# Performance work log

Hardware: AMD Instinct MI355X
Metric: run time of the kernel (lower is better)

Reference implementation:

```python
import jax, jax.numpy as jnp
import numpy as np

N = 100000      # user + item nodes
E = 600000      # number of edges
LATDIM = 128
HEAD = 4
HDIM = LATDIM // HEAD


def setup_inputs() -> dict:
    key = jax.random.key(0)
    ks = jax.random.split(key, 7)
    return {
        "embeds": jax.random.normal(ks[0], (N, LATDIM), dtype=jnp.float32),
        "qTrans": jax.random.normal(ks[1], (LATDIM, LATDIM), dtype=jnp.float32) * (1.0 / np.sqrt(LATDIM)),
        "kTrans": jax.random.normal(ks[2], (LATDIM, LATDIM), dtype=jnp.float32) * (1.0 / np.sqrt(LATDIM)),
        "vTrans": jax.random.normal(ks[3], (LATDIM, LATDIM), dtype=jnp.float32) * (1.0 / np.sqrt(LATDIM)),
        "filt": jax.random.normal(ks[4], (N, HEAD), dtype=jnp.float32),
        "rows": jax.random.randint(ks[5], (E,), 0, N, dtype=jnp.int32),
        "cols": jax.random.randint(ks[6], (E,), 0, N, dtype=jnp.int32),
    }


def reference(embeds, qTrans, kTrans, vTrans, filt, rows, cols):
    # gather endpoint embeddings: [E, latdim]
    rowEmbeds = embeds[rows]
    colEmbeds = embeds[cols]
    # per-edge multi-head q/k/v: [E, H, D]
    qEmbeds = (rowEmbeds @ qTrans).reshape(E, HEAD, HDIM)
    kEmbeds = (colEmbeds @ kTrans).reshape(E, HEAD, HDIM)
    vEmbeds = (colEmbeds @ vTrans).reshape(E, HEAD, HDIM)
    # per-edge per-head attention logits
    att = jnp.einsum('ehd,ehd->eh', qEmbeds, kEmbeds)
    att = jnp.clip(att, -10.0, 10.0)
    att = att + filt[cols]
    expAtt = jnp.exp(att)
    # segment softmax over destination rows
    attNorm = jax.ops.segment_sum(expAtt, rows, num_segments=N)[rows]
    att = expAtt / (attNorm + 1e-8)
    # weighted values, scatter-sum back to nodes
    resEdges = (att[:, :, None] * vEmbeds).reshape(E, LATDIM)
    resEmbeds = jax.ops.segment_sum(resEdges, rows, num_segments=N)
    return resEmbeds
```

## Files before the change

### kernel.cpp

```cpp
#include <hip/hip_runtime.h>

#define N_NODES 100000
#define E_EDGES 600000
#define LATDIM 128
#define HEAD 4
#define HDIM 32

#define SCAN_CHUNK 1024
#define SCAN_NB ((N_NODES + SCAN_CHUNK - 1) / SCAN_CHUNK)

typedef __bf16 bf16x8 __attribute__((ext_vector_type(8)));
typedef float  f32x4  __attribute__((ext_vector_type(4)));

__device__ __forceinline__ unsigned f32_to_bf16_rne(float x) {
    unsigned u = __float_as_uint(x);
    u += 0x7fffu + ((u >> 16) & 1u);
    return u >> 16;
}

__device__ __forceinline__ void bf16_split(float x, unsigned& hi, unsigned& lo) {
    unsigned hb = f32_to_bf16_rne(x);
    float hf = __uint_as_float(hb << 16);
    unsigned lb = f32_to_bf16_rne(x - hf);
    hi = hb; lo = lb;
}

__global__ __launch_bounds__(256) void wprep_kernel(
    const float* __restrict__ qT, const float* __restrict__ kT,
    const float* __restrict__ vT,
    unsigned short* __restrict__ WThi, unsigned short* __restrict__ WTlo)
{
    int g = blockIdx.x * 256 + threadIdx.x;
    if (g >= 3072) return;
    int m    = g >> 10;
    int rem  = g & 1023;
    int c    = rem >> 3;
    int k0   = (rem & 7) * 16;
    const float* W = (m == 0) ? qT : (m == 1) ? kT : vT;

    unsigned short hi[16], lo[16];
    #pragma unroll
    for (int j = 0; j < 16; ++j) {
        float x = W[(size_t)(k0 + j) * 128 + c];
        unsigned hb, lb;
        bf16_split(x, hb, lb);
        hi[j] = (unsigned short)hb;
        lo[j] = (unsigned short)lb;
    }
    size_t off = (size_t)m * 16384 + (size_t)c * 128 + k0;
    *(uint4*)(WThi + off)     = *(const uint4*)&hi[0];
    *(uint4*)(WThi + off + 8) = *(const uint4*)&hi[8];
    *(uint4*)(WTlo + off)     = *(const uint4*)&lo[0];
    *(uint4*)(WTlo + off + 8) = *(const uint4*)&lo[8];
}

__global__ __launch_bounds__(256, 4) void qkv_mfma_kernel(
    const float* __restrict__ embeds,
    const unsigned short* __restrict__ WThi,
    const unsigned short* __restrict__ WTlo,
    float* __restrict__ Q, unsigned* __restrict__ KV)
{
    __shared__ __align__(16) char smem[32768];
    char* Ahi = smem;
    char* Alo = smem + 16384;
    char* Bhi = smem;
    char* Blo = smem + 16384;

    const int tid = threadIdx.x;
    const int rowBase = blockIdx.x * 64;

    uint4 pbh0, pbh1, pbh2, pbh3;
    uint4 pbl0, pbl1, pbl2, pbl3;

#define PF(MN, HN) do {                                                          \
        const char* _sh = (const char*)(WThi + (size_t)(MN) * 16384 + (size_t)(HN) * 8192); \
        const char* _sl = (const char*)(WTlo + (size_t)(MN) * 16384 + (size_t)(HN) * 8192); \
        pbh0 = *(const uint4*)(_sh + (size_t)(0 * 256 + tid) * 16);              \
        pbh1 = *(const uint4*)(_sh + (size_t)(1 * 256 + tid) * 16);              \
        pbh2 = *(const uint4*)(_sh + (size_t)(2 * 256 + tid) * 16);              \
        pbh3 = *(const uint4*)(_sh + (size_t)(3 * 256 + tid) * 16);              \
        pbl0 = *(const uint4*)(_sl + (size_t)(0 * 256 + tid) * 16);              \
        pbl1 = *(const uint4*)(_sl + (size_t)(1 * 256 + tid) * 16);              \
        pbl2 = *(const uint4*)(_sl + (size_t)(2 * 256 + tid) * 16);              \
        pbl3 = *(const uint4*)(_sl + (size_t)(3 * 256 + tid) * 16);              \
    } while (0)

#define COMMIT() do {                                                            \
        { int _i = 0 * 256 + tid; int _c = _i >> 4;                              \
          int _s = (_c * 256 + (_i & 15) * 16) ^ ((_c & 7) << 4);                \
          *(uint4*)(Bhi + _s) = pbh0; *(uint4*)(Blo + _s) = pbl0; }              \
        { int _i = 1 * 256 + tid; int _c = _i >> 4;                              \
          int _s = (_c * 256 + (_i & 15) * 16) ^ ((_c & 7) << 4);                \
          *(uint4*)(Bhi + _s) = pbh1; *(uint4*)(Blo + _s) = pbl1; }              \
        { int _i = 2 * 256 + tid; int _c = _i >> 4;                              \
          int _s = (_c * 256 + (_i & 15) * 16) ^ ((_c & 7) << 4);                \
          *(uint4*)(Bhi + _s) = pbh2; *(uint4*)(Blo + _s) = pbl2; }              \
        { int _i = 3 * 256 + tid; int _c = _i >> 4;                              \
          int _s = (_c * 256 + (_i & 15) * 16) ^ ((_c & 7) << 4);                \
          *(uint4*)(Bhi + _s) = pbh3; *(uint4*)(Blo + _s) = pbl3; }              \
    } while (0)

#define MFMA_PANEL(ACC) do {                                                     \
        _Pragma("unroll")                                                        \
        for (int kk = 0; kk < 4; ++kk) {                                         \
            _Pragma("unroll")                                                    \
            for (int n = 0; n < 4; ++n) {                                        \
                int brow = n * 16 + lrow;                                        \
                int byte = brow * 256 + kk * 64 + kg * 16;                       \
                int swz  = byte ^ ((lrow & 7) << 4);                             \
                bf16x8 bh = __builtin_bit_cast(bf16x8, *(const uint4*)(Bhi + swz)); \
                bf16x8 bl = __builtin_bit_cast(bf16x8, *(const uint4*)(Blo + swz)); \
                ACC[n] = __builtin_amdgcn_mfma_f32_16x16x32_bf16(a_hi[kk], bh, ACC[n], 0, 0, 0); \
                ACC[n] = __builtin_amdgcn_mfma_f32_16x16x32_bf16(a_lo[kk], bh, ACC[n], 0, 0, 0); \
                ACC[n] = __builtin_amdgcn_mfma_f32_16x16x32_bf16(a_hi[kk], bl, ACC[n], 0, 0, 0); \
            }                                                                    \
        }                                                                        \
    } while (0)

#define ZACC(ACC) f32x4 ACC[4] = { {0.f,0.f,0.f,0.f}, {0.f,0.f,0.f,0.f},         \
                                   {0.f,0.f,0.f,0.f}, {0.f,0.f,0.f,0.f} }

#define STORE_Q(ACC, H) do {                                                     \
        _Pragma("unroll")                                                        \
        for (int n = 0; n < 4; ++n)                                              \
        _Pragma("unroll")                                                        \
        for (int j = 0; j < 4; ++j) {                                            \
            int gr  = rowBase + wv * 16 + orow + j;                              \
            int col = (H) * 64 + n * 16 + lrow;                                  \
            if (gr < N_NODES) Q[(size_t)gr * 128 + col] = ACC[n][j];             \
        }                                                                        \
    } while (0)

#define STORE_KV(ACC, H) do {                                                    \
        _Pragma("unroll")                                                        \
        for (int n = 0; n < 4; ++n)                                              \
        _Pragma("unroll")                                                        \
        for (int j = 0; j < 4; ++j) {                                            \
            int gr  = rowBase + wv * 16 + orow + j;                              \
            int col = (H) * 64 + n * 16 + lrow;                                  \
            if (gr < N_NODES) {                                                  \
                unsigned pk = f32_to_bf16_rne(kreg[n][j])                        \
                            | (f32_to_bf16_rne(ACC[n][j]) << 16);                \
                KV[(size_t)gr * 128 + col] = pk;                                 \
            }                                                                    \
        }                                                                        \
    } while (0)

    PF(0, 0);

    #pragma unroll
    for (int it = 0; it < 8; ++it) {
        int idx = it * 256 + tid;
        int r  = idx >> 5;
        int c4 = idx & 31;
        int gr = rowBase + r;
        float4 v = make_float4(0.f, 0.f, 0.f, 0.f);
        if (gr < N_NODES) v = ((const float4*)embeds)[(size_t)gr * 32 + c4];
        unsigned hx, lx, hy, ly, hz, lz, hw, lw;
        bf16_split(v.x, hx, lx); bf16_split(v.y, hy, ly);
        bf16_split(v.z, hz, lz); bf16_split(v.w, hw, lw);
        uint2 hp = make_uint2(hx | (hy << 16), hz | (hw << 16));
        uint2 lp = make_uint2(lx | (ly << 16), lz | (lw << 16));
        int byte = r * 256 + c4 * 8;
        int swz  = byte ^ ((r & 7) << 4);
        *(uint2*)(Ahi + swz) = hp;
        *(uint2*)(Alo + swz) = lp;
    }
    __syncthreads();

    const int lane = tid & 63;
    const int wv   = tid >> 6;
    const int lrow = lane & 15;
    const int kg   = lane >> 4;
    const int arow = wv * 16 + lrow;
    const int orow = kg << 2;

    bf16x8 a_hi[4], a_lo[4];
    #pragma unroll
    for (int kk = 0; kk < 4; ++kk) {
        int byte = arow * 256 + kk * 64 + kg * 16;
        int swz  = byte ^ ((lrow & 7) << 4);
        a_hi[kk] = __builtin_bit_cast(bf16x8, *(const uint4*)(Ahi + swz));
        a_lo[kk] = __builtin_bit_cast(bf16x8, *(const uint4*)(Alo + swz));
    }
    __syncthreads();

    COMMIT();
    __syncthreads();

    f32x4 kreg[4];

    {
        PF(1, 0);
        ZACC(acc);
        MFMA_PANEL(acc);
        STORE_Q(acc, 0);
        __syncthreads(); COMMIT(); __syncthreads();
    }
    {
        PF(2, 0);
        ZACC(acc);
        MFMA_PANEL(acc);
        kreg[0] = acc[0]; kreg[1] = acc[1]; kreg[2] = acc[2]; kreg[3] = acc[3];
        __syncthreads(); COMMIT(); __syncthreads();
    }
    {
        PF(0, 1);
        ZACC(acc);
        MFMA_PANEL(acc);
        STORE_KV(acc, 0);
        __syncthreads(); COMMIT(); __syncthreads();
    }
    {
        PF(1, 1);
        ZACC(acc);
        MFMA_PANEL(acc);
        STORE_Q(acc, 1);
        __syncthreads(); COMMIT(); __syncthreads();
    }
    {
        PF(2, 1);
        ZACC(acc);
        MFMA_PANEL(acc);
        kreg[0] = acc[0]; kreg[1] = acc[1]; kreg[2] = acc[2]; kreg[3] = acc[3];
        __syncthreads(); COMMIT(); __syncthreads();
    }
    {
        ZACC(acc);
        MFMA_PANEL(acc);
        STORE_KV(acc, 1);
    }

#undef PF
#undef COMMIT
#undef MFMA_PANEL
#undef ZACC
#undef STORE_Q
#undef STORE_KV
}

__global__ __launch_bounds__(256) void hist_kernel(
    const int* __restrict__ rows, int* __restrict__ counts)
{
    int e = blockIdx.x * 256 + threadIdx.x;
    if (e < E_EDGES) atomicAdd(&counts[rows[e]], 1);
}

__global__ __launch_bounds__(256) void scan1_kernel(
    const int* __restrict__ counts, int* __restrict__ starts,
    int* __restrict__ blockSums)
{
    __shared__ int s[256];
    int b = blockIdx.x, t = threadIdx.x;
    int base = b * SCAN_CHUNK + t * 4;
    int v0 = (base + 0 < N_NODES) ? counts[base + 0] : 0;
    int v1 = (base + 1 < N_NODES) ? counts[base + 1] : 0;
    int v2 = (base + 2 < N_NODES) ? counts[base + 2] : 0;
    int v3 = (base + 3 < N_NODES) ? counts[base + 3] : 0;
    int local = v0 + v1 + v2 + v3;
    s[t] = local;
    __syncthreads();
    for (int off = 1; off < 256; off <<= 1) {
        int x = (t >= off) ? s[t - off] : 0;
        __syncthreads();
        s[t] += x;
        __syncthreads();
    }
    int incl = s[t];
    int excl = incl - local;
    if (base + 0 < N_NODES) starts[base + 0] = excl;
    if (base + 1 < N_NODES) starts[base + 1] = excl + v0;
    if (base + 2 < N_NODES) starts[base + 2] = excl + v0 + v1;
    if (base + 3 < N_NODES) starts[base + 3] = excl + v0 + v1 + v2;
    if (t == 255) blockSums[b] = incl;
}

__global__ __launch_bounds__(128) void scan2_kernel(int* __restrict__ blockSums)
{
    __shared__ int s[128];
    int t = threadIdx.x;
    int v = (t < SCAN_NB) ? blockSums[t] : 0;
    s[t] = v;
    __syncthreads();
    for (int off = 1; off < 128; off <<= 1) {
        int x = (t >= off) ? s[t - off] : 0;
        __syncthreads();
        s[t] += x;
        __syncthreads();
    }
    if (t < SCAN_NB) blockSums[t] = s[t] - v;
}

__global__ __launch_bounds__(256) void scan3_kernel(
    int* __restrict__ starts, const int* __restrict__ blockSums,
    int* __restrict__ cursor)
{
    int i = blockIdx.x * 256 + threadIdx.x;
    if (i < N_NODES) {
        int v = starts[i] + blockSums[i >> 10];
        starts[i] = v;
        cursor[i] = v;
    }
}

__global__ __launch_bounds__(256) void scatter_kernel(
    const int* __restrict__ rows, const int* __restrict__ cols,
    int* __restrict__ cursor, int* __restrict__ csrCols)
{
    int e = blockIdx.x * 256 + threadIdx.x;
    if (e >= E_EDGES) return;
    int pos = atomicAdd(&cursor[rows[e]], 1);
    csrCols[pos] = cols[e];
}

__global__ __launch_bounds__(256) void att_agg_kernel(
    const float* __restrict__ Q, const unsigned* __restrict__ KV,
    const float* __restrict__ filt,
    const int* __restrict__ starts, const int* __restrict__ counts,
    const int* __restrict__ csrCols,
    float* __restrict__ out)
{
    int t = threadIdx.x;
    int node = blockIdx.x * 8 + (t >> 5);
    if (node >= N_NODES) return;
    int lane = t & 31;
    int h = lane >> 3;

    float4 q = ((const float4*)(Q + (size_t)node * 128))[lane];
    int s   = starts[node];
    int cnt = counts[node];

    float norm = 0.f;
    float ax = 0.f, ay = 0.f, az = 0.f, aw = 0.f;

    int i = 0;
    for (; i + 2 <= cnt; i += 2) {
        int c0 = csrCols[s + i];
        int c1 = csrCols[s + i + 1];
        uint4 kv0 = ((const uint4*)KV)[(size_t)c0 * 32 + lane];
        uint4 kv1 = ((const uint4*)KV)[(size_t)c1 * 32 + lane];
        float f0 = filt[c0 * HEAD + h];
        float f1 = filt[c1 * HEAD + h];

        float k0x = __uint_as_float(kv0.x << 16), v0x = __uint_as_float(kv0.x & 0xffff0000u);
        float k0y = __uint_as_float(kv0.y << 16), v0y = __uint_as_float(kv0.y & 0xffff0000u);
        float k0z = __uint_as_float(kv0.z << 16), v0z = __uint_as_float(kv0.z & 0xffff0000u);
        float k0w = __uint_as_float(kv0.w << 16), v0w = __uint_as_float(kv0.w & 0xffff0000u);
        float k1x = __uint_as_float(kv1.x << 16), v1x = __uint_as_float(kv1.x & 0xffff0000u);
        float k1y = __uint_as_float(kv1.y << 16), v1y = __uint_as_float(kv1.y & 0xffff0000u);
        float k1z = __uint_as_float(kv1.z << 16), v1z = __uint_as_float(kv1.z & 0xffff0000u);
        float k1w = __uint_as_float(kv1.w << 16), v1w = __uint_as_float(kv1.w & 0xffff0000u);

        float p0 = q.x * k0x + q.y * k0y + q.z * k0z + q.w * k0w;
        float p1 = q.x * k1x + q.y * k1y + q.z * k1z + q.w * k1w;
        p0 += __shfl_xor(p0, 1);   p1 += __shfl_xor(p1, 1);
        p0 += __shfl_xor(p0, 2);   p1 += __shfl_xor(p1, 2);
        p0 += __shfl_xor(p0, 4);   p1 += __shfl_xor(p1, 4);

        float w0 = __expf(fminf(fmaxf(p0, -10.f), 10.f) + f0);
        float w1 = __expf(fminf(fmaxf(p1, -10.f), 10.f) + f1);
        norm += w0 + w1;
        ax += w0 * v0x + w1 * v1x;
        ay += w0 * v0y + w1 * v1y;
        az += w0 * v0z + w1 * v1z;
        aw += w0 * v0w + w1 * v1w;
    }
    if (i < cnt) {
        int c0 = csrCols[s + i];
        uint4 kv0 = ((const uint4*)KV)[(size_t)c0 * 32 + lane];
        float f0 = filt[c0 * HEAD + h];
        float k0x = __uint_as_float(kv0.x << 16), v0x = __uint_as_float(kv0.x & 0xffff0000u);
        float k0y = __uint_as_float(kv0.y << 16), v0y = __uint_as_float(kv0.y & 0xffff0000u);
        float k0z = __uint_as_float(kv0.z << 16), v0z = __uint_as_float(kv0.z & 0xffff0000u);
        float k0w = __uint_as_float(kv0.w << 16), v0w = __uint_as_float(kv0.w & 0xffff0000u);
        float p0 = q.x * k0x + q.y * k0y + q.z * k0z + q.w * k0w;
        p0 += __shfl_xor(p0, 1);
        p0 += __shfl_xor(p0, 2);
        p0 += __shfl_xor(p0, 4);
        float w0 = __expf(fminf(fmaxf(p0, -10.f), 10.f) + f0);
        norm += w0;
        ax += w0 * v0x; ay += w0 * v0y; az += w0 * v0z; aw += w0 * v0w;
    }
    float inv = 1.0f / (norm + 1e-8f);
    ((float4*)(out + (size_t)node * 128))[lane] =
        make_float4(ax * inv, ay * inv, az * inv, aw * inv);
}

extern "C" void kernel_launch(void* const* d_in, const int* in_sizes, int n_in,
                              void* d_out, int out_size, void* d_ws, size_t ws_size,
                              hipStream_t stream) {
    const float* embeds = (const float*)d_in[0];
    const float* qT     = (const float*)d_in[1];
    const float* kT     = (const float*)d_in[2];
    const float* vT     = (const float*)d_in[3];
    const float* filt   = (const float*)d_in[4];
    const int*   rows   = (const int*)d_in[5];
    const int*   cols   = (const int*)d_in[6];
    float*       out    = (float*)d_out;

    float*    Q  = (float*)d_ws;
    unsigned* KV = (unsigned*)(Q + (size_t)N_NODES * 128);
    int* counts    = (int*)(KV + (size_t)N_NODES * 128);
    int* starts    = counts + N_NODES;
    int* cursor    = starts + N_NODES;
    int* blockSums = cursor + N_NODES;
    int* csrCols   = blockSums + 128;

    unsigned short* WThi = (unsigned short*)csrCols;
    unsigned short* WTlo = WThi + 3 * 128 * 128;

    hipMemsetAsync(counts, 0, sizeof(int) * N_NODES, stream);

    wprep_kernel<<<12, 256, 0, stream>>>(qT, kT, vT, WThi, WTlo);
    qkv_mfma_kernel<<<(N_NODES + 63) / 64, 256, 0, stream>>>(embeds, WThi, WTlo, Q, KV);

    hist_kernel<<<(E_EDGES + 255) / 256, 256, 0, stream>>>(rows, counts);
    scan1_kernel<<<SCAN_NB, 256, 0, stream>>>(counts, starts, blockSums);
    scan2_kernel<<<1, 128, 0, stream>>>(blockSums);
    scan3_kernel<<<(N_NODES + 255) / 256, 256, 0, stream>>>(starts, blockSums, cursor);
    scatter_kernel<<<(E_EDGES + 255) / 256, 256, 0, stream>>>(rows, cols, cursor, csrCols);

    att_agg_kernel<<<(N_NODES + 7) / 8, 256, 0, stream>>>(
        Q, KV, filt, starts, counts, csrCols, out);
}
```

Before: 295.2 us.

## Fuse histogram into QKV GEMM, single-pass scan, double-buffer weight panels

Counts zeroing moves into the weight-prep kernel, the edge histogram is folded into the QKV MFMA kernel, and the three-kernel scan becomes one decoupled look-back scan that also writes the cursor. The aim is to cut kernel launches and the memset. The QKV kernel now uses 512-thread blocks over 128 rows with double-buffered B panels in 64KB LDS, which removes one barrier per panel. The look-back scan relies on blocks being scheduled in order to avoid spinning forever. The state array sits after csrCols, beyond the old workspace layout.

```diff
diff --git a/kernel.cpp b/kernel.cpp
--- a/kernel.cpp
+++ b/kernel.cpp
@@ -6,8 +6,7 @@
 #define HEAD 4
 #define HDIM 32
 
-#define SCAN_CHUNK 1024
-#define SCAN_NB ((N_NODES + SCAN_CHUNK - 1) / SCAN_CHUNK)
+#define SCAN_NB 98
 
 typedef __bf16 bf16x8 __attribute__((ext_vector_type(8)));
 typedef float  f32x4  __attribute__((ext_vector_type(4)));
@@ -28,9 +27,14 @@
 __global__ __launch_bounds__(256) void wprep_kernel(
     const float* __restrict__ qT, const float* __restrict__ kT,
     const float* __restrict__ vT,
-    unsigned short* __restrict__ WThi, unsigned short* __restrict__ WTlo)
+    unsigned short* __restrict__ WThi, unsigned short* __restrict__ WTlo,
+    int* __restrict__ counts, unsigned* __restrict__ state)
 {
     int g = blockIdx.x * 256 + threadIdx.x;
+
+    for (int i = g; i < N_NODES; i += SCAN_NB * 256) counts[i] = 0;
+    if (g < 128) state[g] = 0u;
+
     if (g >= 3072) return;
     int m    = g >> 10;
     int rem  = g & 1023;
@@ -54,53 +58,46 @@
     *(uint4*)(WTlo + off + 8) = *(const uint4*)&lo[8];
 }
 
-__global__ __launch_bounds__(256, 4) void qkv_mfma_kernel(
+__global__ __launch_bounds__(512, 2) void qkv_mfma_kernel(
     const float* __restrict__ embeds,
     const unsigned short* __restrict__ WThi,
     const unsigned short* __restrict__ WTlo,
+    const int* __restrict__ rows,
+    int* __restrict__ counts,
     float* __restrict__ Q, unsigned* __restrict__ KV)
 {
-    __shared__ __align__(16) char smem[32768];
+    __shared__ __align__(16) char smem[65536];
     char* Ahi = smem;
-    char* Alo = smem + 16384;
-    char* Bhi = smem;
-    char* Blo = smem + 16384;
+    char* Alo = smem + 32768;
+    char* B0h = smem;
+    char* B0l = smem + 16384;
+    char* B1h = smem + 32768;
+    char* B1l = smem + 49152;
 
     const int tid = threadIdx.x;
-    const int rowBase = blockIdx.x * 64;
-
-    uint4 pbh0, pbh1, pbh2, pbh3;
-    uint4 pbl0, pbl1, pbl2, pbl3;
+    const int rowBase = blockIdx.x * 128;
+
+    uint4 pbh0, pbh1, pbl0, pbl1;
 
 #define PF(MN, HN) do {                                                          \
         const char* _sh = (const char*)(WThi + (size_t)(MN) * 16384 + (size_t)(HN) * 8192); \
         const char* _sl = (const char*)(WTlo + (size_t)(MN) * 16384 + (size_t)(HN) * 8192); \
-        pbh0 = *(const uint4*)(_sh + (size_t)(0 * 256 + tid) * 16);              \
-        pbh1 = *(const uint4*)(_sh + (size_t)(1 * 256 + tid) * 16);              \
-        pbh2 = *(const uint4*)(_sh + (size_t)(2 * 256 + tid) * 16);              \
-        pbh3 = *(const uint4*)(_sh + (size_t)(3 * 256 + tid) * 16);              \
-        pbl0 = *(const uint4*)(_sl + (size_t)(0 * 256 + tid) * 16);              \
-        pbl1 = *(const uint4*)(_sl + (size_t)(1 * 256 + tid) * 16);              \
-        pbl2 = *(const uint4*)(_sl + (size_t)(2 * 256 + tid) * 16);              \
-        pbl3 = *(const uint4*)(_sl + (size_t)(3 * 256 + tid) * 16);              \
+        pbh0 = *(const uint4*)(_sh + (size_t)tid * 16);                          \
+        pbh1 = *(const uint4*)(_sh + (size_t)(512 + tid) * 16);                  \
+        pbl0 = *(const uint4*)(_sl + (size_t)tid * 16);                          \
+        pbl1 = *(const uint4*)(_sl + (size_t)(512 + tid) * 16);                  \
     } while (0)
 
-#define COMMIT() do {                                                            \
-        { int _i = 0 * 256 + tid; int _c = _i >> 4;                              \
+#define COMMIT(BHI, BLO) do {                                                    \
+        { int _i = tid; int _c = _i >> 4;                                        \
           int _s = (_c * 256 + (_i & 15) * 16) ^ ((_c & 7) << 4);                \
-          *(uint4*)(Bhi + _s) = pbh0; *(uint4*)(Blo + _s) = pbl0; }              \
-        { int _i = 1 * 256 + tid; int _c = _i >> 4;                              \
+          *(uint4*)((BHI) + _s) = pbh0; *(uint4*)((BLO) + _s) = pbl0; }          \
+        { int _i = 512 + tid; int _c = _i >> 4;                                  \
           int _s = (_c * 256 + (_i & 15) * 16) ^ ((_c & 7) << 4);                \
-          *(uint4*)(Bhi + _s) = pbh1; *(uint4*)(Blo + _s) = pbl1; }              \
-        { int _i = 2 * 256 + tid; int _c = _i >> 4;                              \
-          int _s = (_c * 256 + (_i & 15) * 16) ^ ((_c & 7) << 4);                \
-          *(uint4*)(Bhi + _s) = pbh2; *(uint4*)(Blo + _s) = pbl2; }              \
-        { int _i = 3 * 256 + tid; int _c = _i >> 4;                              \
-          int _s = (_c * 256 + (_i & 15) * 16) ^ ((_c & 7) << 4);                \
-          *(uint4*)(Bhi + _s) = pbh3; *(uint4*)(Blo + _s) = pbl3; }              \
+          *(uint4*)((BHI) + _s) = pbh1; *(uint4*)((BLO) + _s) = pbl1; }          \
     } while (0)
 
-#define MFMA_PANEL(ACC) do {                                                     \
+#define MFMA_PANEL(ACC, BHI, BLO) do {                                           \
         _Pragma("unroll")                                                        \
         for (int kk = 0; kk < 4; ++kk) {                                         \
             _Pragma("unroll")                                                    \
@@ -108,8 +105,8 @@
                 int brow = n * 16 + lrow;                                        \
                 int byte = brow * 256 + kk * 64 + kg * 16;                       \
                 int swz  = byte ^ ((lrow & 7) << 4);                             \
-                bf16x8 bh = __builtin_bit_cast(bf16x8, *(const uint4*)(Bhi + swz)); \
-                bf16x8 bl = __builtin_bit_cast(bf16x8, *(const uint4*)(Blo + swz)); \
+                bf16x8 bh = __builtin_bit_cast(bf16x8, *(const uint4*)((BHI) + swz)); \
+                bf16x8 bl = __builtin_bit_cast(bf16x8, *(const uint4*)((BLO) + swz)); \
                 ACC[n] = __builtin_amdgcn_mfma_f32_16x16x32_bf16(a_hi[kk], bh, ACC[n], 0, 0, 0); \
                 ACC[n] = __builtin_amdgcn_mfma_f32_16x16x32_bf16(a_lo[kk], bh, ACC[n], 0, 0, 0); \
                 ACC[n] = __builtin_amdgcn_mfma_f32_16x16x32_bf16(a_hi[kk], bl, ACC[n], 0, 0, 0); \
@@ -148,9 +145,12 @@
 
     PF(0, 0);
 
+    for (int e = blockIdx.x * 512 + tid; e < E_EDGES; e += gridDim.x * 512)
+        atomicAdd(&counts[rows[e]], 1);
+
     #pragma unroll
     for (int it = 0; it < 8; ++it) {
-        int idx = it * 256 + tid;
+        int idx = it * 512 + tid;
         int r  = idx >> 5;
         int c4 = idx & 31;
         int gr = rowBase + r;
@@ -185,49 +185,44 @@
     }
     __syncthreads();
 
-    COMMIT();
+    COMMIT(B0h, B0l);
     __syncthreads();
 
     f32x4 kreg[4];
 
     {
-        PF(1, 0);
+        PF(1, 0); ZACC(acc);
+        MFMA_PANEL(acc, B0h, B0l);
+        STORE_Q(acc, 0);
+        COMMIT(B1h, B1l); __syncthreads();
+    }
+    {
+        PF(2, 0); ZACC(acc);
+        MFMA_PANEL(acc, B1h, B1l);
+        kreg[0] = acc[0]; kreg[1] = acc[1]; kreg[2] = acc[2]; kreg[3] = acc[3];
+        COMMIT(B0h, B0l); __syncthreads();
+    }
+    {
+        PF(0, 1); ZACC(acc);
+        MFMA_PANEL(acc, B0h, B0l);
+        STORE_KV(acc, 0);
+        COMMIT(B1h, B1l); __syncthreads();
+    }
+    {
+        PF(1, 1); ZACC(acc);
+        MFMA_PANEL(acc, B1h, B1l);
+        STORE_Q(acc, 1);
+        COMMIT(B0h, B0l); __syncthreads();
+    }
+    {
+        PF(2, 1); ZACC(acc);
+        MFMA_PANEL(acc, B0h, B0l);
+        kreg[0] = acc[0]; kreg[1] = acc[1]; kreg[2] = acc[2]; kreg[3] = acc[3];
+        COMMIT(B1h, B1l); __syncthreads();
+    }
+    {
         ZACC(acc);
-        MFMA_PANEL(acc);
-        STORE_Q(acc, 0);
-        __syncthreads(); COMMIT(); __syncthreads();
-    }
-    {
-        PF(2, 0);
-        ZACC(acc);
-        MFMA_PANEL(acc);
-        kreg[0] = acc[0]; kreg[1] = acc[1]; kreg[2] = acc[2]; kreg[3] = acc[3];
-        __syncthreads(); COMMIT(); __syncthreads();
-    }
-    {
-        PF(0, 1);
-        ZACC(acc);
-        MFMA_PANEL(acc);
-        STORE_KV(acc, 0);
-        __syncthreads(); COMMIT(); __syncthreads();
-    }
-    {
-        PF(1, 1);
-        ZACC(acc);
-        MFMA_PANEL(acc);
-        STORE_Q(acc, 1);
-        __syncthreads(); COMMIT(); __syncthreads();
-    }
-    {
-        PF(2, 1);
-        ZACC(acc);
-        MFMA_PANEL(acc);
-        kreg[0] = acc[0]; kreg[1] = acc[1]; kreg[2] = acc[2]; kreg[3] = acc[3];
-        __syncthreads(); COMMIT(); __syncthreads();
-    }
-    {
-        ZACC(acc);
-        MFMA_PANEL(acc);
+        MFMA_PANEL(acc, B1h, B1l);
         STORE_KV(acc, 1);
     }
 
@@ -239,20 +234,14 @@
 #undef STORE_KV
 }
 
-__global__ __launch_bounds__(256) void hist_kernel(
-    const int* __restrict__ rows, int* __restrict__ counts)
-{
-    int e = blockIdx.x * 256 + threadIdx.x;
-    if (e < E_EDGES) atomicAdd(&counts[rows[e]], 1);
-}
-
-__global__ __launch_bounds__(256) void scan1_kernel(
+__global__ __launch_bounds__(256) void scan_lb_kernel(
     const int* __restrict__ counts, int* __restrict__ starts,
-    int* __restrict__ blockSums)
+    int* __restrict__ cursor, unsigned* __restrict__ state)
 {
     __shared__ int s[256];
+    __shared__ int bcast;
     int b = blockIdx.x, t = threadIdx.x;
-    int base = b * SCAN_CHUNK + t * 4;
+    int base = b * 1024 + t * 4;
     int v0 = (base + 0 < N_NODES) ? counts[base + 0] : 0;
     int v1 = (base + 1 < N_NODES) ? counts[base + 1] : 0;
     int v2 = (base + 2 < N_NODES) ? counts[base + 2] : 0;
@@ -266,41 +255,35 @@
         s[t] += x;
         __syncthreads();
     }
-    int incl = s[t];
-    int excl = incl - local;
-    if (base + 0 < N_NODES) starts[base + 0] = excl;
-    if (base + 1 < N_NODES) starts[base + 1] = excl + v0;
-    if (base + 2 < N_NODES) starts[base + 2] = excl + v0 + v1;
-    if (base + 3 < N_NODES) starts[base + 3] = excl + v0 + v1 + v2;
-    if (t == 255) blockSums[b] = incl;
-}
-
-__global__ __launch_bounds__(128) void scan2_kernel(int* __restrict__ blockSums)
-{
-    __shared__ int s[128];
-    int t = threadIdx.x;
-    int v = (t < SCAN_NB) ? blockSums[t] : 0;
-    s[t] = v;
+    int incl  = s[t];
+    int excl  = incl - local;
+    int total = s[255];
+
+    if (t == 0) {
+        int sum = 0;
+        if (b == 0) {
+            atomicExch(&state[0], ((unsigned)total << 2) | 2u);
+        } else {
+            atomicExch(&state[b], ((unsigned)total << 2) | 1u);
+            int i = b - 1;
+            while (true) {
+                unsigned w = atomicAdd(&state[i], 0u);
+                unsigned st = w & 3u;
+                if (st == 0u) continue;
+                sum += (int)(w >> 2);
+                if (st == 2u) break;
+                --i;
+            }
+            atomicExch(&state[b], ((unsigned)(sum + total) << 2) | 2u);
+        }
+        bcast = sum;
+    }
     __syncthreads();
-    for (int off = 1; off < 128; off <<= 1) {
-        int x = (t >= off) ? s[t - off] : 0;
-        __syncthreads();
-        s[t] += x;
-        __syncthreads();
-    }
-    if (t < SCAN_NB) blockSums[t] = s[t] - v;
-}
-
-__global__ __launch_bounds__(256) void scan3_kernel(
-    int* __restrict__ starts, const int* __restrict__ blockSums,
-    int* __restrict__ cursor)
-{
-    int i = blockIdx.x * 256 + threadIdx.x;
-    if (i < N_NODES) {
-        int v = starts[i] + blockSums[i >> 10];
-        starts[i] = v;
-        cursor[i] = v;
-    }
+    int e = excl + bcast;
+    if (base + 0 < N_NODES) { starts[base + 0] = e;                cursor[base + 0] = e; }
+    if (base + 1 < N_NODES) { starts[base + 1] = e + v0;           cursor[base + 1] = e + v0; }
+    if (base + 2 < N_NODES) { starts[base + 2] = e + v0 + v1;      cursor[base + 2] = e + v0 + v1; }
+    if (base + 3 < N_NODES) { starts[base + 3] = e + v0 + v1 + v2; cursor[base + 3] = e + v0 + v1 + v2; }
 }
 
 __global__ __launch_bounds__(256) void scatter_kernel(
@@ -403,23 +386,17 @@
     int* counts    = (int*)(KV + (size_t)N_NODES * 128);
     int* starts    = counts + N_NODES;
     int* cursor    = starts + N_NODES;
-    int* blockSums = cursor + N_NODES;
-    int* csrCols   = blockSums + 128;
+    int* csrCols   = cursor + N_NODES;
+    unsigned* state = (unsigned*)(csrCols + E_EDGES);
 
     unsigned short* WThi = (unsigned short*)csrCols;
     unsigned short* WTlo = WThi + 3 * 128 * 128;
 
-    hipMemsetAsync(counts, 0, sizeof(int) * N_NODES, stream);
-
-    wprep_kernel<<<12, 256, 0, stream>>>(qT, kT, vT, WThi, WTlo);
-    qkv_mfma_kernel<<<(N_NODES + 63) / 64, 256, 0, stream>>>(embeds, WThi, WTlo, Q, KV);
-
-    hist_kernel<<<(E_EDGES + 255) / 256, 256, 0, stream>>>(rows, counts);
-    scan1_kernel<<<SCAN_NB, 256, 0, stream>>>(counts, starts, blockSums);
-    scan2_kernel<<<1, 128, 0, stream>>>(blockSums);
-    scan3_kernel<<<(N_NODES + 255) / 256, 256, 0, stream>>>(starts, blockSums, cursor);
+    wprep_kernel<<<SCAN_NB, 256, 0, stream>>>(qT, kT, vT, WThi, WTlo, counts, state);
+    qkv_mfma_kernel<<<(N_NODES + 127) / 128, 512, 0, stream>>>(
+        embeds, WThi, WTlo, rows, counts, Q, KV);
+    scan_lb_kernel<<<SCAN_NB, 256, 0, stream>>>(counts, starts, cursor, state);
     scatter_kernel<<<(E_EDGES + 255) / 256, 256, 0, stream>>>(rows, cols, cursor, csrCols);
-
     att_agg_kernel<<<(N_NODES + 7) / 8, 256, 0, stream>>>(
         Q, KV, filt, starts, counts, csrCols, out);
 }
```

New measurement: 272.4 us. 1.08x faster.

## Fuse memset, histogram and three-pass scan into fewer kernels with decoupled lookback

Applied to the files above, without the earlier changes.

Zeroing of counts moves into the weight-prep kernel, the edge histogram atomics move to the tail of the QKV MFMA kernel, and the three-kernel scan becomes a single-pass decoupled-lookback scan that also writes the cursor array. This removes a memset and four launches plus their inter-kernel gaps. It also relaxes the QKV kernel's occupancy hint to waves_per_eu(2,4). The lookback spin relies on all 98 scan blocks being co-resident, and WThi/WTlo still alias csrCols while the state array is placed after it.

```diff
diff --git a/kernel.cpp b/kernel.cpp
--- a/kernel.cpp
+++ b/kernel.cpp
@@ -6,8 +6,7 @@
 #define HEAD 4
 #define HDIM 32
 
-#define SCAN_CHUNK 1024
-#define SCAN_NB ((N_NODES + SCAN_CHUNK - 1) / SCAN_CHUNK)
+#define SCAN_NB 98
 
 typedef __bf16 bf16x8 __attribute__((ext_vector_type(8)));
 typedef float  f32x4  __attribute__((ext_vector_type(4)));
@@ -28,9 +27,14 @@
 __global__ __launch_bounds__(256) void wprep_kernel(
     const float* __restrict__ qT, const float* __restrict__ kT,
     const float* __restrict__ vT,
-    unsigned short* __restrict__ WThi, unsigned short* __restrict__ WTlo)
+    unsigned short* __restrict__ WThi, unsigned short* __restrict__ WTlo,
+    int* __restrict__ counts, unsigned* __restrict__ state)
 {
     int g = blockIdx.x * 256 + threadIdx.x;
+
+    for (int i = g; i < N_NODES; i += SCAN_NB * 256) counts[i] = 0;
+    if (g < 128) state[g] = 0u;
+
     if (g >= 3072) return;
     int m    = g >> 10;
     int rem  = g & 1023;
@@ -54,10 +58,14 @@
     *(uint4*)(WTlo + off + 8) = *(const uint4*)&lo[8];
 }
 
-__global__ __launch_bounds__(256, 4) void qkv_mfma_kernel(
+__global__ __launch_bounds__(256)
+__attribute__((amdgpu_waves_per_eu(2, 4)))
+void qkv_mfma_kernel(
     const float* __restrict__ embeds,
     const unsigned short* __restrict__ WThi,
     const unsigned short* __restrict__ WTlo,
+    const int* __restrict__ rows,
+    int* __restrict__ counts,
     float* __restrict__ Q, unsigned* __restrict__ KV)
 {
     __shared__ __align__(16) char smem[32768];
@@ -231,6 +239,9 @@
         STORE_KV(acc, 1);
     }
 
+    for (int e = blockIdx.x * 256 + tid; e < E_EDGES; e += gridDim.x * 256)
+        atomicAdd(&counts[rows[e]], 1);
+
 #undef PF
 #undef COMMIT
 #undef MFMA_PANEL
@@ -239,20 +250,14 @@
 #undef STORE_KV
 }
 
-__global__ __launch_bounds__(256) void hist_kernel(
-    const int* __restrict__ rows, int* __restrict__ counts)
-{
-    int e = blockIdx.x * 256 + threadIdx.x;
-    if (e < E_EDGES) atomicAdd(&counts[rows[e]], 1);
-}
-
-__global__ __launch_bounds__(256) void scan1_kernel(
+__global__ __launch_bounds__(256) void scan_lb_kernel(
     const int* __restrict__ counts, int* __restrict__ starts,
-    int* __restrict__ blockSums)
+    int* __restrict__ cursor, unsigned* __restrict__ state)
 {
     __shared__ int s[256];
+    __shared__ int bcast;
     int b = blockIdx.x, t = threadIdx.x;
-    int base = b * SCAN_CHUNK + t * 4;
+    int base = b * 1024 + t * 4;
     int v0 = (base + 0 < N_NODES) ? counts[base + 0] : 0;
     int v1 = (base + 1 < N_NODES) ? counts[base + 1] : 0;
     int v2 = (base + 2 < N_NODES) ? counts[base + 2] : 0;
@@ -266,41 +271,35 @@
         s[t] += x;
         __syncthreads();
     }
-    int incl = s[t];
-    int excl = incl - local;
-    if (base + 0 < N_NODES) starts[base + 0] = excl;
-    if (base + 1 < N_NODES) starts[base + 1] = excl + v0;
-    if (base + 2 < N_NODES) starts[base + 2] = excl + v0 + v1;
-    if (base + 3 < N_NODES) starts[base + 3] = excl + v0 + v1 + v2;
-    if (t == 255) blockSums[b] = incl;
-}
-
-__global__ __launch_bounds__(128) void scan2_kernel(int* __restrict__ blockSums)
-{
-    __shared__ int s[128];
-    int t = threadIdx.x;
-    int v = (t < SCAN_NB) ? blockSums[t] : 0;
-    s[t] = v;
+    int incl  = s[t];
+    int excl  = incl - local;
+    int total = s[255];
+
+    if (t == 0) {
+        int sum = 0;
+        if (b == 0) {
+            atomicExch(&state[0], ((unsigned)total << 2) | 2u);
+        } else {
+            atomicExch(&state[b], ((unsigned)total << 2) | 1u);
+            int i = b - 1;
+            while (true) {
+                unsigned w = atomicAdd(&state[i], 0u);
+                unsigned st = w & 3u;
+                if (st == 0u) continue;
+                sum += (int)(w >> 2);
+                if (st == 2u) break;
+                --i;
+            }
+            atomicExch(&state[b], ((unsigned)(sum + total) << 2) | 2u);
+        }
+        bcast = sum;
+    }
     __syncthreads();
-    for (int off = 1; off < 128; off <<= 1) {
-        int x = (t >= off) ? s[t - off] : 0;
-        __syncthreads();
-        s[t] += x;
-        __syncthreads();
-    }
-    if (t < SCAN_NB) blockSums[t] = s[t] - v;
-}
-
-__global__ __launch_bounds__(256) void scan3_kernel(
-    int* __restrict__ starts, const int* __restrict__ blockSums,
-    int* __restrict__ cursor)
-{
-    int i = blockIdx.x * 256 + threadIdx.x;
-    if (i < N_NODES) {
-        int v = starts[i] + blockSums[i >> 10];
-        starts[i] = v;
-        cursor[i] = v;
-    }
+    int e = excl + bcast;
+    if (base + 0 < N_NODES) { starts[base + 0] = e;                cursor[base + 0] = e; }
+    if (base + 1 < N_NODES) { starts[base + 1] = e + v0;           cursor[base + 1] = e + v0; }
+    if (base + 2 < N_NODES) { starts[base + 2] = e + v0 + v1;      cursor[base + 2] = e + v0 + v1; }
+    if (base + 3 < N_NODES) { starts[base + 3] = e + v0 + v1 + v2; cursor[base + 3] = e + v0 + v1 + v2; }
 }
 
 __global__ __launch_bounds__(256) void scatter_kernel(
@@ -403,23 +402,17 @@
     int* counts    = (int*)(KV + (size_t)N_NODES * 128);
     int* starts    = counts + N_NODES;
     int* cursor    = starts + N_NODES;
-    int* blockSums = cursor + N_NODES;
-    int* csrCols   = blockSums + 128;
+    int* csrCols   = cursor + N_NODES;
+    unsigned* state = (unsigned*)(csrCols + E_EDGES);
 
     unsigned short* WThi = (unsigned short*)csrCols;
     unsigned short* WTlo = WThi + 3 * 128 * 128;
 
-    hipMemsetAsync(counts, 0, sizeof(int) * N_NODES, stream);
-
-    wprep_kernel<<<12, 256, 0, stream>>>(qT, kT, vT, WThi, WTlo);
-    qkv_mfma_kernel<<<(N_NODES + 63) / 64, 256, 0, stream>>>(embeds, WThi, WTlo, Q, KV);
-
-    hist_kernel<<<(E_EDGES + 255) / 256, 256, 0, stream>>>(rows, counts);
-    scan1_kernel<<<SCAN_NB, 256, 0, stream>>>(counts, starts, blockSums);
-    scan2_kernel<<<1, 128, 0, stream>>>(blockSums);
-    scan3_kernel<<<(N_NODES + 255) / 256, 256, 0, stream>>>(starts, blockSums, cursor);
+    wprep_kernel<<<SCAN_NB, 256, 0, stream>>>(qT, kT, vT, WThi, WTlo, counts, state);
+    qkv_mfma_kernel<<<(N_NODES + 63) / 64, 256, 0, stream>>>(
+        embeds, WThi, WTlo, rows, counts, Q, KV);
+    scan_lb_kernel<<<SCAN_NB, 256, 0, stream>>>(counts, starts, cursor, state);
     scatter_kernel<<<(E_EDGES + 255) / 256, 256, 0, stream>>>(rows, cols, cursor, csrCols);
-
     att_agg_kernel<<<(N_NODES + 7) / 8, 256, 0, stream>>>(
         Q, KV, filt, starts, counts, csrCols, out);
 }
```

New measurement: 271.7 us. -8.0%, faster.
